# Optimization experiments

Hardware: AMD Instinct MI355X
Metric: run time of the kernel (lower is better)

The kernel has to match this reference:

```python
import jax, jax.numpy as jnp
import numpy as np

N_NODE = 20000
N_EDGE = 200000
EMBED = 256
PAIR = 128
HEADS = 16
HEAD_DIM = EMBED // HEADS
SCALING = HEAD_DIM ** -0.5
EPS = 1e-5


def _ln(x, w, b):
    m = x.mean(-1, keepdims=True)
    v = ((x - m) ** 2).mean(-1, keepdims=True)
    return (x - m) / jnp.sqrt(v + EPS) * w + b


def setup_inputs() -> dict:
    key = jax.random.key(0)
    ks = jax.random.split(key, 12)
    inp = {
        "query": jax.random.normal(ks[0], (N_NODE, EMBED), jnp.float32),
        "edge_index": jax.random.randint(ks[1], (N_EDGE, 2), 0, N_NODE, jnp.int64 if jax.config.jax_enable_x64 else jnp.int32),
        "edge_diff": jax.random.normal(ks[2], (N_EDGE, 3), jnp.float32),
        "pair": jax.random.normal(ks[3], (N_EDGE, PAIR), jnp.float32),
        "ln_w": jnp.ones((EMBED,), jnp.float32),
        "ln_b": jnp.zeros((EMBED,), jnp.float32),
        "pln_w": jnp.ones((PAIR,), jnp.float32),
        "pln_b": jnp.zeros((PAIR,), jnp.float32),
        "Wq": jax.random.normal(ks[4], (EMBED, EMBED), jnp.float32) * 0.02,
        "Wk": jax.random.normal(ks[5], (EMBED, EMBED), jnp.float32) * 0.02,
        "Wv": jax.random.normal(ks[6], (EMBED, EMBED), jnp.float32) * 0.02,
        "Wb": jax.random.normal(ks[7], (HEADS, PAIR), jnp.float32) * 0.02,
        "bb": jnp.zeros((HEADS,), jnp.float32),
        "Wf1": jax.random.normal(ks[8], (1, EMBED), jnp.float32) * 0.02,
        "bf1": jnp.zeros((1,), jnp.float32),
        "Wf2": jax.random.normal(ks[9], (1, EMBED), jnp.float32) * 0.02,
        "bf2": jnp.zeros((1,), jnp.float32),
        "Wf3": jax.random.normal(ks[10], (1, EMBED), jnp.float32) * 0.02,
        "bf3": jnp.zeros((1,), jnp.float32),
    }
    return inp


def reference(query, edge_index, edge_diff, pair, ln_w, ln_b, pln_w, pln_b,
              Wq, Wk, Wv, Wb, bb, Wf1, bf1, Wf2, bf2, Wf3, bf3):
    n_node = query.shape[0]
    src = edge_index[:, 0]
    dst = edge_index[:, 1]

    qn = _ln(query, ln_w, ln_b)          # preln on node features
    pn = _ln(pair, pln_w, pln_b)         # preln on pair features

    q = (qn @ Wq.T).reshape(n_node, HEADS, HEAD_DIM)
    k = (qn @ Wk.T).reshape(n_node, HEADS, HEAD_DIM)
    v = (qn @ Wv.T).reshape(n_node, HEADS, HEAD_DIM)

    qe = q[src] * SCALING                # [E,H,D]
    ke = k[dst]
    ve = v[dst]

    logits = (qe * ke).sum(-1) + pn @ Wb.T + bb   # [E,H]

    # segment softmax over destination node (edge_index[:,0])
    seg_max = jax.ops.segment_max(logits, src, num_segments=n_node)  # [N,H]
    ex = jnp.exp(logits - seg_max[src])
    denom = jax.ops.segment_sum(ex, src, num_segments=n_node)
    probs = ex / denom[src]              # [E,H]

    # 3D-weighted scatter-sum: out[n,h,c,d] = sum_e probs[e,h]*diff[e,c]*v[e,h,d]
    w = probs[:, :, None] * edge_diff[:, None, :]                    # [E,H,3]
    contrib = w[:, :, :, None] * ve[:, :, None, :]                   # [E,H,3,D]
    x = jax.ops.segment_sum(contrib, src, num_segments=n_node)       # [N,H,3,D]
    x = x.transpose(0, 2, 1, 3).reshape(n_node, 3, EMBED)            # [N,3,H*D]

    f1 = x[:, 0, :] @ Wf1.T + bf1
    f2 = x[:, 1, :] @ Wf2.T + bf2
    f3 = x[:, 2, :] @ Wf3.T + bf3
    return jnp.concatenate([f1, f2, f3], axis=-1).astype(jnp.float32)
```

## Files before the change

kernel.cpp:

```cpp
#include <hip/hip_runtime.h>
#include <math.h>

#define N_NODE 20000
#define N_EDGE 200000
#define EMBED 256
#define PAIR 128
#define HEADS 16
#define HEAD_DIM 16
#define SCALING 0.25f
#define LNEPS 1e-5f

typedef unsigned short u16;
typedef unsigned int u32;
typedef __attribute__((ext_vector_type(8))) short bf16x8;
typedef __attribute__((ext_vector_type(4))) float f32x4;

#define WS_QKV   0
#define WS_QN    20480000
#define WS_WBF   30720000
#define WS_WW    31047680
#define WS_C0    31051776
#define WS_C1    31051840
#define WS_BIAS  31051904
#define WS_VW    43851904
#define WS_CNT   47691904
#define WS_CUR   47771904
#define WS_OFF   47851904
#define WS_DE    47931968

__device__ __forceinline__ u16 f2bf(float f) {
  u32 u = __float_as_uint(f);
  u32 r = (u + 0x7FFFu + ((u >> 16) & 1u)) >> 16;
  return (u16)r;
}
__device__ __forceinline__ float bl(u32 u) { return __uint_as_float(u << 16); }
__device__ __forceinline__ float bh(u32 u) { return __uint_as_float(u & 0xFFFF0000u); }

__device__ __forceinline__ float dot8(uint4 a, uint4 b) {
  float s = bl(a.x) * bl(b.x) + bh(a.x) * bh(b.x);
  s += bl(a.y) * bl(b.y) + bh(a.y) * bh(b.y);
  s += bl(a.z) * bl(b.z) + bh(a.z) * bh(b.z);
  s += bl(a.w) * bl(b.w) + bh(a.w) * bh(b.w);
  return s;
}

__global__ __launch_bounds__(256) void k1_pre_hist_kernel(
    const float* __restrict__ query, const float* __restrict__ ln_w,
    const float* __restrict__ ln_b, u16* __restrict__ qn,
    const float* __restrict__ Wq, const float* __restrict__ Wk,
    const float* __restrict__ Wv, u16* __restrict__ WbfAll,
    const float* __restrict__ pln_w, const float* __restrict__ pln_b,
    const float* __restrict__ Wb, const float* __restrict__ bb,
    u16* __restrict__ WWbf, float* __restrict__ c0, float* __restrict__ c1,
    const float* __restrict__ Wf1, const float* __restrict__ Wf2,
    const float* __restrict__ Wf3, const int* __restrict__ edge_index,
    int* __restrict__ counts) {
  int bid = blockIdx.x;
  int t = threadIdx.x;
  if (bid < 5000) {
    int node = bid * 4 + (t >> 6);
    int lane = t & 63;
    float4 a = *(const float4*)(query + (size_t)node * EMBED + lane * 4);
    float s = a.x + a.y + a.z + a.w;
    float s2 = a.x * a.x + a.y * a.y + a.z * a.z + a.w * a.w;
    #pragma unroll
    for (int off = 32; off > 0; off >>= 1) {
      s += __shfl_xor(s, off);
      s2 += __shfl_xor(s2, off);
    }
    float m = s * (1.0f / EMBED);
    float r = rsqrtf(s2 * (1.0f / EMBED) - m * m + LNEPS);
    float4 w4 = *(const float4*)(ln_w + lane * 4);
    float4 b4 = *(const float4*)(ln_b + lane * 4);
    ushort4 st;
    st.x = f2bf((a.x - m) * r * w4.x + b4.x);
    st.y = f2bf((a.y - m) * r * w4.y + b4.y);
    st.z = f2bf((a.z - m) * r * w4.z + b4.z);
    st.w = f2bf((a.w - m) * r * w4.w + b4.w);
    *(ushort4*)(qn + (size_t)node * EMBED + lane * 4) = st;
  } else if (bid < 5128) {
    int g4 = (bid - 5000) * 256 + t;
    int idx = g4 * 4;
    const float* src = (idx < 65536) ? Wq : Wk;
    float4 v = *(const float4*)(src + (idx & 65535));
    ushort4 st = {f2bf(v.x), f2bf(v.y), f2bf(v.z), f2bf(v.w)};
    *(ushort4*)(WbfAll + idx) = st;
  } else if (bid == 5128) {
    if (t < 64) {
      int l = t;
      for (int h = 0; h < HEADS; h++) {
        int i0 = l * 2;
        float wb0 = Wb[h * PAIR + i0], wb1 = Wb[h * PAIR + i0 + 1];
        float ww0 = pln_w[i0] * wb0, ww1 = pln_w[i0 + 1] * wb1;
        WWbf[h * PAIR + i0] = f2bf(ww0);
        WWbf[h * PAIR + i0 + 1] = f2bf(ww1);
        float s1 = ww0 + ww1;
        float s0 = pln_b[i0] * wb0 + pln_b[i0 + 1] * wb1;
        #pragma unroll
        for (int off = 32; off > 0; off >>= 1) {
          s1 += __shfl_xor(s1, off);
          s0 += __shfl_xor(s0, off);
        }
        if (l == 0) {
          c1[h] = s1;
          c0[h] = s0 + bb[h];
        }
      }
    }
  } else if (bid == 5129) {
    for (int j = 0; j < 48; j++) {
      int h = j / 3, c = j - h * 3;
      const float* wf = (c == 0) ? Wf1 : ((c == 1) ? Wf2 : Wf3);
      float s = 0.f;
      #pragma unroll
      for (int d = 0; d < 16; d++)
        s += Wv[(size_t)(h * 16 + d) * 256 + t] * wf[h * 16 + d];
      WbfAll[(size_t)(512 + j) * 256 + t] = f2bf(s);
    }
    for (int r = 0; r < 80; r++) WbfAll[(size_t)(560 + r) * 256 + t] = 0;
  } else {
    int e = (bid - 5130) * 256 + t;
    if (e < N_EDGE) atomicAdd(&counts[edge_index[e * 2]], 1);
  }
}

#define BKP 72
__global__ __launch_bounds__(256, 2) void k2_gemm_scan_kernel(
    const u16* __restrict__ qn, const u16* __restrict__ WbfAll,
    u16* __restrict__ qkv, float* __restrict__ vw,
    const int* __restrict__ counts, int* __restrict__ off) {
  int bid = blockIdx.x;
  int t = threadIdx.x;
  if (bid == 785) {
    __shared__ int part[256];
    int i0 = t * 79;
    int i1 = i0 + 79; if (i1 > N_NODE) i1 = N_NODE;
    int s = 0;
    for (int i = i0; i < i1; i++) s += counts[i];
    part[t] = s;
    __syncthreads();
    int x = s;
    for (int o = 1; o < 256; o <<= 1) {
      int y = (t >= o) ? part[t - o] : 0;
      __syncthreads();
      x += y;
      part[t] = x;
      __syncthreads();
    }
    int run = x - s;
    for (int i = i0; i < i1; i++) {
      off[i] = run;
      run += counts[i];
    }
    if (t == 255) off[N_NODE] = N_EDGE;
    return;
  }
  __shared__ u16 As[128 * BKP];
  __shared__ u16 Bs[128 * BKP];
  int bx = bid % 157, by = bid / 157;
  int wv = t >> 6, lane = t & 63;
  int quad = lane >> 4, l16 = lane & 15;
  int row0 = bx * 128, col0 = by * 128;
  int mt = (wv >> 1) * 64, nt = (wv & 1) * 64;

  f32x4 acc[4][4];
  #pragma unroll
  for (int im = 0; im < 4; im++)
    #pragma unroll
    for (int in_ = 0; in_ < 4; in_++) acc[im][in_] = (f32x4){0.f, 0.f, 0.f, 0.f};

  for (int it = 0; it < 4; it++) {
    int k0 = it * 64;
    #pragma unroll
    for (int j = 0; j < 4; j++) {
      int L = j * 256 + t;
      int row = L >> 3, slot = L & 7;
      int ra = min(row0 + row, N_NODE - 1);
      uint4 va = *(const uint4*)(qn + (size_t)ra * 256 + k0 + slot * 8);
      *(uint4*)(&As[row * BKP + slot * 8]) = va;
      uint4 vb = *(const uint4*)(WbfAll + (size_t)(col0 + row) * 256 + k0 + slot * 8);
      *(uint4*)(&Bs[row * BKP + slot * 8]) = vb;
    }
    __syncthreads();
    #pragma unroll
    for (int s = 0; s < 2; s++) {
      int ko = s * 32 + quad * 8;
      bf16x8 af[4], bf[4];
      #pragma unroll
      for (int im = 0; im < 4; im++)
        af[im] = *(const bf16x8*)(&As[(mt + im * 16 + l16) * BKP + ko]);
      #pragma unroll
      for (int in_ = 0; in_ < 4; in_++)
        bf[in_] = *(const bf16x8*)(&Bs[(nt + in_ * 16 + l16) * BKP + ko]);
      #pragma unroll
      for (int im = 0; im < 4; im++)
        #pragma unroll
        for (int in_ = 0; in_ < 4; in_++)
          acc[im][in_] = __builtin_amdgcn_mfma_f32_16x16x32_bf16(
              af[im], bf[in_], acc[im][in_], 0, 0, 0);
    }
    __syncthreads();
  }
  #pragma unroll
  for (int im = 0; im < 4; im++) {
    #pragma unroll
    for (int in_ = 0; in_ < 4; in_++) {
      int gcol = col0 + nt + in_ * 16 + l16;
      float scale = (gcol < 256) ? SCALING : 1.0f;
      #pragma unroll
      for (int r = 0; r < 4; r++) {
        int grow = row0 + mt + im * 16 + quad * 4 + r;
        if (grow < N_NODE) {
          if (gcol < 512) {
            qkv[(size_t)grow * 512 + gcol] = f2bf(acc[im][in_][r] * scale);
          } else if (gcol < 560) {
            vw[(size_t)grow * 48 + (gcol - 512)] = acc[im][in_][r];
          }
        }
      }
    }
  }
}

#define PP 136
__global__ __launch_bounds__(256) void k3_bias_scatter_kernel(
    const float* __restrict__ pair, const u16* __restrict__ WWbf,
    const float* __restrict__ c0g, const float* __restrict__ c1g,
    float* __restrict__ bias, const int* __restrict__ edge_index,
    const int* __restrict__ off, int* __restrict__ cur,
    int2* __restrict__ de) {
  __shared__ u16 Ps[64 * PP];
  __shared__ u16 WWs[16 * PP];
  __shared__ float ms[64], rs[64], c0s[16], c1s[16];
  int bid = blockIdx.x;
  int t = threadIdx.x;
  int wv = t >> 6, lane = t & 63;
  int quad = lane >> 4, l16 = lane & 15;
  int e0 = bid * 64;
  #pragma unroll
  for (int j = 0; j < 8; j++) {
    int L = j * 256 + t;
    int row = L >> 5, slot = L & 31;
    float4 p = *(const float4*)(pair + (size_t)(e0 + row) * PAIR + slot * 4);
    ushort4 st = {f2bf(p.x), f2bf(p.y), f2bf(p.z), f2bf(p.w)};
    *(ushort4*)(&Ps[row * PP + slot * 4]) = st;
  }
  #pragma unroll
  for (int j = 0; j < 2; j++) {
    int L = j * 256 + t;
    int row = L >> 5, slot = L & 31;
    ushort4 w = *(const ushort4*)(WWbf + row * PAIR + slot * 4);
    *(ushort4*)(&WWs[row * PP + slot * 4]) = w;
  }
  if (t < 16) {
    c0s[t] = c0g[t];
    c1s[t] = c1g[t];
  }
  if (t < 64) {
    int e = e0 + t;
    int srcn = edge_index[e * 2 + 0];
    int dstn = edge_index[e * 2 + 1];
    int pos = off[srcn] + atomicAdd(&cur[srcn], 1);
    de[pos] = make_int2(dstn, e);
  }
  __syncthreads();
  {
    int row = t >> 2, qq = t & 3;
    float s = 0.f, s2 = 0.f;
    #pragma unroll
    for (int jj = 0; jj < 8; jj++) {
      ushort4 u = *(const ushort4*)(&Ps[row * PP + (qq * 8 + jj) * 4]);
      float x0 = __uint_as_float((u32)u.x << 16);
      float x1 = __uint_as_float((u32)u.y << 16);
      float x2 = __uint_as_float((u32)u.z << 16);
      float x3 = __uint_as_float((u32)u.w << 16);
      s += x0 + x1 + x2 + x3;
      s2 += x0 * x0 + x1 * x1 + x2 * x2 + x3 * x3;
    }
    s += __shfl_xor(s, 1); s += __shfl_xor(s, 2);
    s2 += __shfl_xor(s2, 1); s2 += __shfl_xor(s2, 2);
    if (qq == 0) {
      float m = s * (1.0f / PAIR);
      ms[row] = m;
      rs[row] = rsqrtf(s2 * (1.0f / PAIR) - m * m + LNEPS);
    }
  }
  __syncthreads();
  f32x4 acc = (f32x4){0.f, 0.f, 0.f, 0.f};
  #pragma unroll
  for (int sk = 0; sk < 4; sk++) {
    int ko = sk * 32 + quad * 8;
    bf16x8 a = *(const bf16x8*)(&Ps[(wv * 16 + l16) * PP + ko]);
    bf16x8 b = *(const bf16x8*)(&WWs[l16 * PP + ko]);
    acc = __builtin_amdgcn_mfma_f32_16x16x32_bf16(a, b, acc, 0, 0, 0);
  }
  #pragma unroll
  for (int r = 0; r < 4; r++) {
    int el = wv * 16 + quad * 4 + r;
    float bv = rs[el] * (acc[r] - ms[el] * c1s[l16]) + c0s[l16];
    bias[(size_t)(e0 + el) * HEADS + l16] = bv;
  }
}

__global__ __launch_bounds__(256) void seg_attn_kernel(
    const u16* __restrict__ qkv, const float* __restrict__ bias,
    const int* __restrict__ off, const int2* __restrict__ de,
    const float* __restrict__ vw, const float* __restrict__ edge_diff,
    const float* __restrict__ bf1, const float* __restrict__ bf2,
    const float* __restrict__ bf3, float* __restrict__ out) {
  int wv = threadIdx.x >> 6, lane = threadIdx.x & 63;
  int src = blockIdx.x * 4 + wv;
  int h = lane & 15, eslot = lane >> 4;
  int lo = off[src];
  int deg = off[src + 1] - lo;
  const uint4* qp = (const uint4*)(qkv + (size_t)src * 512 + h * 16);
  uint4 q0 = qp[0], q1 = qp[1];
  float exsum = 0.f, a0 = 0.f, a1 = 0.f, a2 = 0.f;
  for (int ei = eslot; ei < deg; ei += 4) {
    int2 d_e = de[lo + ei];
    const uint4* kp = (const uint4*)(qkv + (size_t)d_e.x * 512 + 256 + h * 16);
    float d = dot8(q0, kp[0]) + dot8(q1, kp[1]);
    float ex = __expf(d + bias[(size_t)d_e.y * HEADS + h]);
    exsum += ex;
    const float* vp = vw + (size_t)d_e.x * 48 + h * 3;
    const float* dp = edge_diff + (size_t)d_e.y * 3;
    a0 += ex * vp[0] * dp[0];
    a1 += ex * vp[1] * dp[1];
    a2 += ex * vp[2] * dp[2];
  }
  exsum += __shfl_xor(exsum, 16);
  exsum += __shfl_xor(exsum, 32);
  float rden = (exsum > 0.f) ? 1.0f / exsum : 0.f;
  a0 *= rden; a1 *= rden; a2 *= rden;
  #pragma unroll
  for (int o = 1; o < 64; o <<= 1) {
    a0 += __shfl_xor(a0, o);
    a1 += __shfl_xor(a1, o);
    a2 += __shfl_xor(a2, o);
  }
  if (lane == 0) {
    out[src * 3 + 0] = a0 + bf1[0];
    out[src * 3 + 1] = a1 + bf2[0];
    out[src * 3 + 2] = a2 + bf3[0];
  }
}

extern "C" void kernel_launch(void* const* d_in, const int* in_sizes, int n_in,
                              void* d_out, int out_size, void* d_ws,
                              size_t ws_size, hipStream_t stream) {
  const float* query      = (const float*)d_in[0];
  const int*   edge_index = (const int*)d_in[1];
  const float* edge_diff  = (const float*)d_in[2];
  const float* pair       = (const float*)d_in[3];
  const float* ln_w       = (const float*)d_in[4];
  const float* ln_b       = (const float*)d_in[5];
  const float* pln_w      = (const float*)d_in[6];
  const float* pln_b      = (const float*)d_in[7];
  const float* Wq         = (const float*)d_in[8];
  const float* Wk         = (const float*)d_in[9];
  const float* Wv         = (const float*)d_in[10];
  const float* Wb         = (const float*)d_in[11];
  const float* bb         = (const float*)d_in[12];
  const float* Wf1        = (const float*)d_in[13];
  const float* bf1        = (const float*)d_in[14];
  const float* Wf2        = (const float*)d_in[15];
  const float* bf2        = (const float*)d_in[16];
  const float* Wf3        = (const float*)d_in[17];
  const float* bf3        = (const float*)d_in[18];

  char* ws = (char*)d_ws;
  u16*   qkv   = (u16*)(ws + WS_QKV);
  u16*   qn    = (u16*)(ws + WS_QN);
  u16*   WbfAll= (u16*)(ws + WS_WBF);
  u16*   WWbf  = (u16*)(ws + WS_WW);
  float* c0    = (float*)(ws + WS_C0);
  float* c1    = (float*)(ws + WS_C1);
  float* bias  = (float*)(ws + WS_BIAS);
  float* vw    = (float*)(ws + WS_VW);
  int*   counts= (int*)(ws + WS_CNT);
  int*   cur   = (int*)(ws + WS_CUR);
  int*   off   = (int*)(ws + WS_OFF);
  int2*  de    = (int2*)(ws + WS_DE);
  float* out   = (float*)d_out;

  hipMemsetAsync(ws + WS_CNT, 0, 160000, stream);
  k1_pre_hist_kernel<<<5912, 256, 0, stream>>>(
      query, ln_w, ln_b, qn, Wq, Wk, Wv, WbfAll, pln_w, pln_b, Wb, bb, WWbf,
      c0, c1, Wf1, Wf2, Wf3, edge_index, counts);
  k2_gemm_scan_kernel<<<786, 256, 0, stream>>>(qn, WbfAll, qkv, vw, counts,
                                               off);
  k3_bias_scatter_kernel<<<3125, 256, 0, stream>>>(
      pair, WWbf, c0, c1, bias, edge_index, off, cur, de);
  seg_attn_kernel<<<N_NODE / 4, 256, 0, stream>>>(qkv, bias, off, de, vw,
                                                  edge_diff, bf1, bf2, bf3,
                                                  out);
}
```

Before: 317.6 us.

## Restage histogram, scan and CSR scatter across kernels; drop memset

Zeroing of counts/cur moves into the first kernel, so the separate memset launch goes away. The edge histogram moves from k1 into extra blocks of the GEMM kernel. The prefix scan moves out of the GEMM kernel into its own single 1024-thread block with per-thread register-local partial sums. The CSR scatter moves out of the 64-edge bias blocks into dedicated trailing blocks with 256 edges each. This rebalances work so the single-block scan no longer sits as a straggler inside the GEMM, at the cost of one extra serial kernel launch.

```diff
diff --git a/kernel.cpp b/kernel.cpp
--- a/kernel.cpp
+++ b/kernel.cpp
@@ -44,20 +44,22 @@
   return s;
 }
 
-__global__ __launch_bounds__(256) void k1_pre_hist_kernel(
+__global__ __launch_bounds__(256) void k1_pre_kernel(
     const float* __restrict__ query, const float* __restrict__ ln_w,
     const float* __restrict__ ln_b, u16* __restrict__ qn,
+    int* __restrict__ counts, int* __restrict__ cur,
     const float* __restrict__ Wq, const float* __restrict__ Wk,
     const float* __restrict__ Wv, u16* __restrict__ WbfAll,
     const float* __restrict__ pln_w, const float* __restrict__ pln_b,
     const float* __restrict__ Wb, const float* __restrict__ bb,
     u16* __restrict__ WWbf, float* __restrict__ c0, float* __restrict__ c1,
     const float* __restrict__ Wf1, const float* __restrict__ Wf2,
-    const float* __restrict__ Wf3, const int* __restrict__ edge_index,
-    int* __restrict__ counts) {
+    const float* __restrict__ Wf3) {
   int bid = blockIdx.x;
   int t = threadIdx.x;
   if (bid < 5000) {
+    int z = bid * 256 + t;
+    if (z < N_NODE) { counts[z] = 0; cur[z] = 0; }
     int node = bid * 4 + (t >> 6);
     int lane = t & 63;
     float4 a = *(const float4*)(query + (size_t)node * EMBED + lane * 4);
@@ -107,7 +109,7 @@
         }
       }
     }
-  } else if (bid == 5129) {
+  } else {
     for (int j = 0; j < 48; j++) {
       int h = j / 3, c = j - h * 3;
       const float* wf = (c == 0) ? Wf1 : ((c == 1) ? Wf2 : Wf3);
@@ -118,46 +120,24 @@
       WbfAll[(size_t)(512 + j) * 256 + t] = f2bf(s);
     }
     for (int r = 0; r < 80; r++) WbfAll[(size_t)(560 + r) * 256 + t] = 0;
-  } else {
-    int e = (bid - 5130) * 256 + t;
-    if (e < N_EDGE) atomicAdd(&counts[edge_index[e * 2]], 1);
   }
 }
 
 #define BKP 72
-__global__ __launch_bounds__(256, 2) void k2_gemm_scan_kernel(
+__global__ __launch_bounds__(256, 2) void k2_gemm_hist_kernel(
     const u16* __restrict__ qn, const u16* __restrict__ WbfAll,
     u16* __restrict__ qkv, float* __restrict__ vw,
-    const int* __restrict__ counts, int* __restrict__ off) {
-  int bid = blockIdx.x;
-  int t = threadIdx.x;
-  if (bid == 785) {
-    __shared__ int part[256];
-    int i0 = t * 79;
-    int i1 = i0 + 79; if (i1 > N_NODE) i1 = N_NODE;
-    int s = 0;
-    for (int i = i0; i < i1; i++) s += counts[i];
-    part[t] = s;
-    __syncthreads();
-    int x = s;
-    for (int o = 1; o < 256; o <<= 1) {
-      int y = (t >= o) ? part[t - o] : 0;
-      __syncthreads();
-      x += y;
-      part[t] = x;
-      __syncthreads();
-    }
-    int run = x - s;
-    for (int i = i0; i < i1; i++) {
-      off[i] = run;
-      run += counts[i];
-    }
-    if (t == 255) off[N_NODE] = N_EDGE;
-    return;
-  }
+    const int* __restrict__ edge_index, int* __restrict__ counts) {
   __shared__ u16 As[128 * BKP];
   __shared__ u16 Bs[128 * BKP];
+  int bid = blockIdx.x;
+  if (bid >= 785) {
+    int e = (bid - 785) * 256 + threadIdx.x;
+    if (e < N_EDGE) atomicAdd(&counts[edge_index[e * 2]], 1);
+    return;
+  }
   int bx = bid % 157, by = bid / 157;
+  int t = threadIdx.x;
   int wv = t >> 6, lane = t & 63;
   int quad = lane >> 4, l16 = lane & 15;
   int row0 = bx * 128, col0 = by * 128;
@@ -222,8 +202,40 @@
   }
 }
 
+__global__ __launch_bounds__(1024) void scan_kernel(
+    const int* __restrict__ counts, int* __restrict__ off) {
+  __shared__ int part[1024];
+  int t = threadIdx.x;
+  int loc[20];
+  int s = 0;
+  #pragma unroll
+  for (int i = 0; i < 20; i++) {
+    int idx = t * 20 + i;
+    int v = (idx < N_NODE) ? counts[idx] : 0;
+    loc[i] = s;
+    s += v;
+  }
+  part[t] = s;
+  __syncthreads();
+  int x = s;
+  for (int o = 1; o < 1024; o <<= 1) {
+    int y = (t >= o) ? part[t - o] : 0;
+    __syncthreads();
+    x += y;
+    part[t] = x;
+    __syncthreads();
+  }
+  int excl = x - s;
+  #pragma unroll
+  for (int i = 0; i < 20; i++) {
+    int idx = t * 20 + i;
+    if (idx < N_NODE) off[idx] = excl + loc[i];
+  }
+  if (t == 0) off[N_NODE] = N_EDGE;
+}
+
 #define PP 136
-__global__ __launch_bounds__(256) void k3_bias_scatter_kernel(
+__global__ __launch_bounds__(256) void k4_bias_scatter_kernel(
     const float* __restrict__ pair, const u16* __restrict__ WWbf,
     const float* __restrict__ c0g, const float* __restrict__ c1g,
     float* __restrict__ bias, const int* __restrict__ edge_index,
@@ -234,6 +246,16 @@
   __shared__ float ms[64], rs[64], c0s[16], c1s[16];
   int bid = blockIdx.x;
   int t = threadIdx.x;
+  if (bid >= 3125) {
+    int e = (bid - 3125) * 256 + t;
+    if (e < N_EDGE) {
+      int src = edge_index[e * 2 + 0];
+      int dst = edge_index[e * 2 + 1];
+      int pos = off[src] + atomicAdd(&cur[src], 1);
+      de[pos] = make_int2(dst, e);
+    }
+    return;
+  }
   int wv = t >> 6, lane = t & 63;
   int quad = lane >> 4, l16 = lane & 15;
   int e0 = bid * 64;
@@ -255,13 +277,6 @@
   if (t < 16) {
     c0s[t] = c0g[t];
     c1s[t] = c1g[t];
-  }
-  if (t < 64) {
-    int e = e0 + t;
-    int srcn = edge_index[e * 2 + 0];
-    int dstn = edge_index[e * 2 + 1];
-    int pos = off[srcn] + atomicAdd(&cur[srcn], 1);
-    de[pos] = make_int2(dstn, e);
   }
   __syncthreads();
   {
@@ -383,13 +398,13 @@
   int2*  de    = (int2*)(ws + WS_DE);
   float* out   = (float*)d_out;
 
-  hipMemsetAsync(ws + WS_CNT, 0, 160000, stream);
-  k1_pre_hist_kernel<<<5912, 256, 0, stream>>>(
-      query, ln_w, ln_b, qn, Wq, Wk, Wv, WbfAll, pln_w, pln_b, Wb, bb, WWbf,
-      c0, c1, Wf1, Wf2, Wf3, edge_index, counts);
-  k2_gemm_scan_kernel<<<786, 256, 0, stream>>>(qn, WbfAll, qkv, vw, counts,
-                                               off);
-  k3_bias_scatter_kernel<<<3125, 256, 0, stream>>>(
+  k1_pre_kernel<<<5130, 256, 0, stream>>>(query, ln_w, ln_b, qn, counts, cur,
+                                          Wq, Wk, Wv, WbfAll, pln_w, pln_b,
+                                          Wb, bb, WWbf, c0, c1, Wf1, Wf2, Wf3);
+  k2_gemm_hist_kernel<<<1567, 256, 0, stream>>>(qn, WbfAll, qkv, vw,
+                                                edge_index, counts);
+  scan_kernel<<<1, 1024, 0, stream>>>(counts, off);
+  k4_bias_scatter_kernel<<<3907, 256, 0, stream>>>(
       pair, WWbf, c0, c1, bias, edge_index, off, cur, de);
   seg_attn_kernel<<<N_NODE / 4, 256, 0, stream>>>(qkv, bias, off, de, vw,
                                                   edge_diff, bf1, bf2, bf3,
```

New measurement: 403.2 us. 1.27x slower.

## Fold pair-bias computation into preprocessing kernel and split out edge scatter

Applied to the files above, without the earlier changes.

Moves the pair layernorm/bias MFMA work out of the third kernel into the first preprocessing kernel as extra blocks. Each bias block now derives the folded Wb weights and c0/c1 constants itself instead of reading them from a workspace. The serial single-block Wf/Wv folding and zero-fill are split across many blocks. The edge CSR scatter becomes its own small kernel. The QKV GEMM K-tile drops from 64 to 32, which reduces shared memory but doubles the number of synchronisation steps. The intent is to overlap bias work with the independent preprocessing and to shorten the critical path through the serial blocks. The cost is redundant per-block weight folding and an extra kernel launch.

```diff
diff --git a/kernel.cpp b/kernel.cpp
--- a/kernel.cpp
+++ b/kernel.cpp
@@ -18,9 +18,6 @@
 #define WS_QKV   0
 #define WS_QN    20480000
 #define WS_WBF   30720000
-#define WS_WW    31047680
-#define WS_C0    31051776
-#define WS_C1    31051840
 #define WS_BIAS  31051904
 #define WS_VW    43851904
 #define WS_CNT   47691904
@@ -44,17 +41,20 @@
   return s;
 }
 
-__global__ __launch_bounds__(256) void k1_pre_hist_kernel(
+#define PP 136
+
+__global__ __launch_bounds__(256) void k1_pre_hist_bias_kernel(
     const float* __restrict__ query, const float* __restrict__ ln_w,
     const float* __restrict__ ln_b, u16* __restrict__ qn,
     const float* __restrict__ Wq, const float* __restrict__ Wk,
     const float* __restrict__ Wv, u16* __restrict__ WbfAll,
     const float* __restrict__ pln_w, const float* __restrict__ pln_b,
     const float* __restrict__ Wb, const float* __restrict__ bb,
-    u16* __restrict__ WWbf, float* __restrict__ c0, float* __restrict__ c1,
     const float* __restrict__ Wf1, const float* __restrict__ Wf2,
     const float* __restrict__ Wf3, const int* __restrict__ edge_index,
-    int* __restrict__ counts) {
+    int* __restrict__ counts, const float* __restrict__ pair,
+    float* __restrict__ bias) {
+  __shared__ u16 smem[11200];
   int bid = blockIdx.x;
   int t = threadIdx.x;
   if (bid < 5000) {
@@ -85,54 +85,121 @@
     float4 v = *(const float4*)(src + (idx & 65535));
     ushort4 st = {f2bf(v.x), f2bf(v.y), f2bf(v.z), f2bf(v.w)};
     *(ushort4*)(WbfAll + idx) = st;
-  } else if (bid == 5128) {
-    if (t < 64) {
-      int l = t;
-      for (int h = 0; h < HEADS; h++) {
-        int i0 = l * 2;
-        float wb0 = Wb[h * PAIR + i0], wb1 = Wb[h * PAIR + i0 + 1];
-        float ww0 = pln_w[i0] * wb0, ww1 = pln_w[i0 + 1] * wb1;
-        WWbf[h * PAIR + i0] = f2bf(ww0);
-        WWbf[h * PAIR + i0 + 1] = f2bf(ww1);
-        float s1 = ww0 + ww1;
-        float s0 = pln_b[i0] * wb0 + pln_b[i0 + 1] * wb1;
-        #pragma unroll
-        for (int off = 32; off > 0; off >>= 1) {
-          s1 += __shfl_xor(s1, off);
-          s0 += __shfl_xor(s0, off);
-        }
-        if (l == 0) {
-          c1[h] = s1;
-          c0[h] = s0 + bb[h];
-        }
-      }
-    }
-  } else if (bid == 5129) {
-    for (int j = 0; j < 48; j++) {
-      int h = j / 3, c = j - h * 3;
-      const float* wf = (c == 0) ? Wf1 : ((c == 1) ? Wf2 : Wf3);
-      float s = 0.f;
-      #pragma unroll
-      for (int d = 0; d < 16; d++)
-        s += Wv[(size_t)(h * 16 + d) * 256 + t] * wf[h * 16 + d];
-      WbfAll[(size_t)(512 + j) * 256 + t] = f2bf(s);
-    }
-    for (int r = 0; r < 80; r++) WbfAll[(size_t)(560 + r) * 256 + t] = 0;
+  } else if (bid < 5176) {
+    int j = bid - 5128;
+    int h = j / 3, c = j - h * 3;
+    const float* wf = (c == 0) ? Wf1 : ((c == 1) ? Wf2 : Wf3);
+    float s = 0.f;
+    #pragma unroll
+    for (int d = 0; d < 16; d++)
+      s += Wv[(size_t)(h * 16 + d) * 256 + t] * wf[h * 16 + d];
+    WbfAll[(size_t)(512 + j) * 256 + t] = f2bf(s);
+  } else if (bid < 5181) {
+    int base = (bid - 5176) * 512 + t * 2;
+    uint4* p = (uint4*)(WbfAll + (size_t)560 * 256);
+    uint4 z4 = {0u, 0u, 0u, 0u};
+    p[base] = z4;
+    p[base + 1] = z4;
+  } else if (bid < 5963) {
+    int e = (bid - 5181) * 256 + t;
+    if (e < N_EDGE) atomicAdd(&counts[edge_index[e * 2]], 1);
   } else {
-    int e = (bid - 5130) * 256 + t;
-    if (e < N_EDGE) atomicAdd(&counts[edge_index[e * 2]], 1);
-  }
-}
-
-#define BKP 72
+    int e0 = (bid - 5963) * 64;
+    u16* Ps = smem;
+    u16* WWs = smem + 64 * PP;
+    float* ms = (float*)(smem + 80 * PP);
+    float* rs = ms + 64;
+    float* c0s = rs + 64;
+    float* c1s = c0s + 16;
+    int wv = t >> 6, lane = t & 63;
+    int quad = lane >> 4, l16 = lane & 15;
+    #pragma unroll
+    for (int j = 0; j < 8; j++) {
+      int L = j * 256 + t;
+      int row = L >> 5, slot = L & 31;
+      float4 p = *(const float4*)(pair + (size_t)(e0 + row) * PAIR + slot * 4);
+      ushort4 st = {f2bf(p.x), f2bf(p.y), f2bf(p.z), f2bf(p.w)};
+      *(ushort4*)(&Ps[row * PP + slot * 4]) = st;
+    }
+    {
+      int h = t >> 4, i0 = (t & 15) * 8;
+      float4 wbA = *(const float4*)(Wb + h * PAIR + i0);
+      float4 wbB = *(const float4*)(Wb + h * PAIR + i0 + 4);
+      float4 pwA = *(const float4*)(pln_w + i0);
+      float4 pwB = *(const float4*)(pln_w + i0 + 4);
+      float4 pbA = *(const float4*)(pln_b + i0);
+      float4 pbB = *(const float4*)(pln_b + i0 + 4);
+      float w0 = pwA.x * wbA.x, w1 = pwA.y * wbA.y;
+      float w2 = pwA.z * wbA.z, w3 = pwA.w * wbA.w;
+      float w4_ = pwB.x * wbB.x, w5 = pwB.y * wbB.y;
+      float w6 = pwB.z * wbB.z, w7 = pwB.w * wbB.w;
+      ushort4 sA = {f2bf(w0), f2bf(w1), f2bf(w2), f2bf(w3)};
+      ushort4 sB = {f2bf(w4_), f2bf(w5), f2bf(w6), f2bf(w7)};
+      *(ushort4*)(&WWs[h * PP + i0]) = sA;
+      *(ushort4*)(&WWs[h * PP + i0 + 4]) = sB;
+      float s1 = w0 + w1 + w2 + w3 + w4_ + w5 + w6 + w7;
+      float s0 = pbA.x * wbA.x + pbA.y * wbA.y + pbA.z * wbA.z + pbA.w * wbA.w
+               + pbB.x * wbB.x + pbB.y * wbB.y + pbB.z * wbB.z + pbB.w * wbB.w;
+      #pragma unroll
+      for (int off = 8; off > 0; off >>= 1) {
+        s1 += __shfl_xor(s1, off);
+        s0 += __shfl_xor(s0, off);
+      }
+      if ((t & 15) == 0) {
+        c1s[h] = s1;
+        c0s[h] = s0 + bb[h];
+      }
+    }
+    __syncthreads();
+    {
+      int row = t >> 2, qq = t & 3;
+      float s = 0.f, s2 = 0.f;
+      #pragma unroll
+      for (int jj = 0; jj < 8; jj++) {
+        ushort4 u = *(const ushort4*)(&Ps[row * PP + (qq * 8 + jj) * 4]);
+        float x0 = __uint_as_float((u32)u.x << 16);
+        float x1 = __uint_as_float((u32)u.y << 16);
+        float x2 = __uint_as_float((u32)u.z << 16);
+        float x3 = __uint_as_float((u32)u.w << 16);
+        s += x0 + x1 + x2 + x3;
+        s2 += x0 * x0 + x1 * x1 + x2 * x2 + x3 * x3;
+      }
+      s += __shfl_xor(s, 1); s += __shfl_xor(s, 2);
+      s2 += __shfl_xor(s2, 1); s2 += __shfl_xor(s2, 2);
+      if (qq == 0) {
+        float m = s * (1.0f / PAIR);
+        ms[row] = m;
+        rs[row] = rsqrtf(s2 * (1.0f / PAIR) - m * m + LNEPS);
+      }
+    }
+    __syncthreads();
+    f32x4 acc = (f32x4){0.f, 0.f, 0.f, 0.f};
+    #pragma unroll
+    for (int sk = 0; sk < 4; sk++) {
+      int ko = sk * 32 + quad * 8;
+      bf16x8 a = *(const bf16x8*)(&Ps[(wv * 16 + l16) * PP + ko]);
+      bf16x8 b = *(const bf16x8*)(&WWs[l16 * PP + ko]);
+      acc = __builtin_amdgcn_mfma_f32_16x16x32_bf16(a, b, acc, 0, 0, 0);
+    }
+    #pragma unroll
+    for (int r = 0; r < 4; r++) {
+      int el = wv * 16 + quad * 4 + r;
+      float bv = rs[el] * (acc[r] - ms[el] * c1s[l16]) + c0s[l16];
+      bias[(size_t)(e0 + el) * HEADS + l16] = bv;
+    }
+  }
+}
+
+#define BKP 40
 __global__ __launch_bounds__(256, 2) void k2_gemm_scan_kernel(
     const u16* __restrict__ qn, const u16* __restrict__ WbfAll,
     u16* __restrict__ qkv, float* __restrict__ vw,
     const int* __restrict__ counts, int* __restrict__ off) {
+  __shared__ u16 smem[10240];
   int bid = blockIdx.x;
   int t = threadIdx.x;
   if (bid == 785) {
-    __shared__ int part[256];
+    int* part = (int*)smem;
     int i0 = t * 79;
     int i1 = i0 + 79; if (i1 > N_NODE) i1 = N_NODE;
     int s = 0;
@@ -155,8 +222,8 @@
     if (t == 255) off[N_NODE] = N_EDGE;
     return;
   }
-  __shared__ u16 As[128 * BKP];
-  __shared__ u16 Bs[128 * BKP];
+  u16* As = smem;
+  u16* Bs = smem + 128 * BKP;
   int bx = bid % 157, by = bid / 157;
   int wv = t >> 6, lane = t & 63;
   int quad = lane >> 4, l16 = lane & 15;
@@ -169,12 +236,12 @@
     #pragma unroll
     for (int in_ = 0; in_ < 4; in_++) acc[im][in_] = (f32x4){0.f, 0.f, 0.f, 0.f};
 
-  for (int it = 0; it < 4; it++) {
-    int k0 = it * 64;
-    #pragma unroll
-    for (int j = 0; j < 4; j++) {
+  for (int it = 0; it < 8; it++) {
+    int k0 = it * 32;
+    #pragma unroll
+    for (int j = 0; j < 2; j++) {
       int L = j * 256 + t;
-      int row = L >> 3, slot = L & 7;
+      int row = L >> 2, slot = L & 3;
       int ra = min(row0 + row, N_NODE - 1);
       uint4 va = *(const uint4*)(qn + (size_t)ra * 256 + k0 + slot * 8);
       *(uint4*)(&As[row * BKP + slot * 8]) = va;
@@ -182,9 +249,8 @@
       *(uint4*)(&Bs[row * BKP + slot * 8]) = vb;
     }
     __syncthreads();
-    #pragma unroll
-    for (int s = 0; s < 2; s++) {
-      int ko = s * 32 + quad * 8;
+    {
+      int ko = quad * 8;
       bf16x8 af[4], bf[4];
       #pragma unroll
       for (int im = 0; im < 4; im++)
@@ -222,83 +288,15 @@
   }
 }
 
-#define PP 136
-__global__ __launch_bounds__(256) void k3_bias_scatter_kernel(
-    const float* __restrict__ pair, const u16* __restrict__ WWbf,
-    const float* __restrict__ c0g, const float* __restrict__ c1g,
-    float* __restrict__ bias, const int* __restrict__ edge_index,
-    const int* __restrict__ off, int* __restrict__ cur,
-    int2* __restrict__ de) {
-  __shared__ u16 Ps[64 * PP];
-  __shared__ u16 WWs[16 * PP];
-  __shared__ float ms[64], rs[64], c0s[16], c1s[16];
-  int bid = blockIdx.x;
-  int t = threadIdx.x;
-  int wv = t >> 6, lane = t & 63;
-  int quad = lane >> 4, l16 = lane & 15;
-  int e0 = bid * 64;
-  #pragma unroll
-  for (int j = 0; j < 8; j++) {
-    int L = j * 256 + t;
-    int row = L >> 5, slot = L & 31;
-    float4 p = *(const float4*)(pair + (size_t)(e0 + row) * PAIR + slot * 4);
-    ushort4 st = {f2bf(p.x), f2bf(p.y), f2bf(p.z), f2bf(p.w)};
-    *(ushort4*)(&Ps[row * PP + slot * 4]) = st;
-  }
-  #pragma unroll
-  for (int j = 0; j < 2; j++) {
-    int L = j * 256 + t;
-    int row = L >> 5, slot = L & 31;
-    ushort4 w = *(const ushort4*)(WWbf + row * PAIR + slot * 4);
-    *(ushort4*)(&WWs[row * PP + slot * 4]) = w;
-  }
-  if (t < 16) {
-    c0s[t] = c0g[t];
-    c1s[t] = c1g[t];
-  }
-  if (t < 64) {
-    int e = e0 + t;
-    int srcn = edge_index[e * 2 + 0];
-    int dstn = edge_index[e * 2 + 1];
-    int pos = off[srcn] + atomicAdd(&cur[srcn], 1);
-    de[pos] = make_int2(dstn, e);
-  }
-  __syncthreads();
-  {
-    int row = t >> 2, qq = t & 3;
-    float s = 0.f, s2 = 0.f;
-    #pragma unroll
-    for (int jj = 0; jj < 8; jj++) {
-      ushort4 u = *(const ushort4*)(&Ps[row * PP + (qq * 8 + jj) * 4]);
-      float x0 = __uint_as_float((u32)u.x << 16);
-      float x1 = __uint_as_float((u32)u.y << 16);
-      float x2 = __uint_as_float((u32)u.z << 16);
-      float x3 = __uint_as_float((u32)u.w << 16);
-      s += x0 + x1 + x2 + x3;
-      s2 += x0 * x0 + x1 * x1 + x2 * x2 + x3 * x3;
-    }
-    s += __shfl_xor(s, 1); s += __shfl_xor(s, 2);
-    s2 += __shfl_xor(s2, 1); s2 += __shfl_xor(s2, 2);
-    if (qq == 0) {
-      float m = s * (1.0f / PAIR);
-      ms[row] = m;
-      rs[row] = rsqrtf(s2 * (1.0f / PAIR) - m * m + LNEPS);
-    }
-  }
-  __syncthreads();
-  f32x4 acc = (f32x4){0.f, 0.f, 0.f, 0.f};
-  #pragma unroll
-  for (int sk = 0; sk < 4; sk++) {
-    int ko = sk * 32 + quad * 8;
-    bf16x8 a = *(const bf16x8*)(&Ps[(wv * 16 + l16) * PP + ko]);
-    bf16x8 b = *(const bf16x8*)(&WWs[l16 * PP + ko]);
-    acc = __builtin_amdgcn_mfma_f32_16x16x32_bf16(a, b, acc, 0, 0, 0);
-  }
-  #pragma unroll
-  for (int r = 0; r < 4; r++) {
-    int el = wv * 16 + quad * 4 + r;
-    float bv = rs[el] * (acc[r] - ms[el] * c1s[l16]) + c0s[l16];
-    bias[(size_t)(e0 + el) * HEADS + l16] = bv;
+__global__ __launch_bounds__(256) void k4_scatter_kernel(
+    const int* __restrict__ edge_index, const int* __restrict__ off,
+    int* __restrict__ cur, int2* __restrict__ de) {
+  int e = blockIdx.x * 256 + threadIdx.x;
+  if (e < N_EDGE) {
+    int src = edge_index[e * 2 + 0];
+    int dst = edge_index[e * 2 + 1];
+    int pos = off[src] + atomicAdd(&cur[src], 1);
+    de[pos] = make_int2(dst, e);
   }
 }
 
@@ -372,9 +370,6 @@
   u16*   qkv   = (u16*)(ws + WS_QKV);
   u16*   qn    = (u16*)(ws + WS_QN);
   u16*   WbfAll= (u16*)(ws + WS_WBF);
-  u16*   WWbf  = (u16*)(ws + WS_WW);
-  float* c0    = (float*)(ws + WS_C0);
-  float* c1    = (float*)(ws + WS_C1);
   float* bias  = (float*)(ws + WS_BIAS);
   float* vw    = (float*)(ws + WS_VW);
   int*   counts= (int*)(ws + WS_CNT);
@@ -384,13 +379,12 @@
   float* out   = (float*)d_out;
 
   hipMemsetAsync(ws + WS_CNT, 0, 160000, stream);
-  k1_pre_hist_kernel<<<5912, 256, 0, stream>>>(
-      query, ln_w, ln_b, qn, Wq, Wk, Wv, WbfAll, pln_w, pln_b, Wb, bb, WWbf,
-      c0, c1, Wf1, Wf2, Wf3, edge_index, counts);
+  k1_pre_hist_bias_kernel<<<9088, 256, 0, stream>>>(
+      query, ln_w, ln_b, qn, Wq, Wk, Wv, WbfAll, pln_w, pln_b, Wb, bb, Wf1,
+      Wf2, Wf3, edge_index, counts, pair, bias);
   k2_gemm_scan_kernel<<<786, 256, 0, stream>>>(qn, WbfAll, qkv, vw, counts,
                                                off);
-  k3_bias_scatter_kernel<<<3125, 256, 0, stream>>>(
-      pair, WWbf, c0, c1, bias, edge_index, off, cur, de);
+  k4_scatter_kernel<<<782, 256, 0, stream>>>(edge_index, off, cur, de);
   seg_attn_kernel<<<N_NODE / 4, 256, 0, stream>>>(qkv, bias, off, de, vw,
                                                   edge_diff, bf1, bf2, bf3,
                                                   out);
```

After: 292.0 us. 1.09x faster.
